# Optimization experiments

Hardware: AMD Instinct MI355X
Metric: run time of the kernel (lower is better)

## Reference

```python
import jax, jax.numpy as jnp
import numpy as np

TOP_K = 2

def setup_inputs() -> dict:
    key = jax.random.key(0)
    ks = jax.random.split(key, 8)
    B, S, H, F, E = 2, 2048, 1024, 2048, 8
    sH = 1.0 / np.sqrt(H)
    sF = 1.0 / np.sqrt(F)
    return {
        "hidden_states": jax.random.normal(ks[0], (B, S, H), jnp.float32),
        "gate_w": jax.random.normal(ks[1], (E, H), jnp.float32) * sH,
        "w_up": jax.random.normal(ks[2], (E, H, F), jnp.float32) * sH,
        "w_gate": jax.random.normal(ks[3], (E, H, F), jnp.float32) * sH,
        "w_down": jax.random.normal(ks[4], (E, F, H), jnp.float32) * sF,
        "b_up": jnp.zeros((E, F), jnp.float32),
        "b_gate": jnp.zeros((E, F), jnp.float32),
        "b_down": jnp.zeros((E, H), jnp.float32),
    }

def reference(hidden_states, gate_w, w_up, w_gate, w_down, b_up, b_gate, b_down):
    # Flatten [B,S,H] -> [N,H]
    H = hidden_states.shape[-1]
    x = hidden_states.reshape(-1, H)                      # [N,H]
    router_logits = x @ gate_w.T                          # [N,E]
    probs = jax.nn.softmax(router_logits.astype(jnp.float32), axis=-1)
    topv, topi = jax.lax.top_k(probs, TOP_K)              # [N,K]
    topv = topv / topv.sum(axis=-1, keepdims=True)
    N, E = router_logits.shape
    # Sparse combine weights: zero except top-k experts (renormalized).
    w_full = jnp.zeros((N, E), probs.dtype).at[jnp.arange(N)[:, None], topi].set(topv)
    w_full = w_full.astype(x.dtype)
    # SwiGLU per expert (dense over E; combine weights zero out non-selected).
    u = jnp.einsum('nh,ehf->nef', x, w_up) + b_up         # [N,E,F]
    v = jnp.einsum('nh,ehf->nef', x, w_gate) + b_gate
    phi = jax.nn.silu(v) * u
    y = jnp.einsum('nef,efh->neh', phi, w_down) + b_down  # [N,E,H]
    out = jnp.einsum('ne,neh->nh', w_full, y)             # [N,H]
    out = out.reshape(hidden_states.shape)
    return out, router_logits.astype(hidden_states.dtype)
```

## Files before the change

kernel.cpp:

```cpp
#include <hip/hip_runtime.h>
#include <hip/hip_bf16.h>
#include <cstdint>
#include <cstddef>

#define N_TOK 4096
#define H_DIM 1024
#define F_DIM 2048
#define E_NUM 8
#define RCAP 10240
#define MAXT 40

typedef __attribute__((ext_vector_type(8))) short bf16x8;
typedef __attribute__((ext_vector_type(4))) float f32x4;

__device__ __forceinline__ float b2f(uint16_t u) {
  return __uint_as_float(((uint32_t)u) << 16);
}
__device__ __forceinline__ uint16_t f2b(float f) {
  uint32_t x = __float_as_uint(f);
  uint32_t r = (x + 0x7fffu + ((x >> 16) & 1u)) >> 16;
  return (uint16_t)r;
}

__device__ __forceinline__ void gl2lds16(const void* g, void* l) {
  __builtin_amdgcn_global_load_lds(
      (const __attribute__((address_space(1))) uint32_t*)g,
      (__attribute__((address_space(3))) uint32_t*)l, 16, 0, 0);
}

__device__ __forceinline__ void stage256(const uint16_t* src, int ldK,
                                         char* lds, int wave, int lane) {
  int u = (lane & 7) ^ (lane >> 3);
  const char* s0 = (const char*)src + u * 16;
  size_t rb = (size_t)ldK * 2;
  int Rb = wave * 32 + (lane >> 3);
  char* d0 = lds + wave * 4096;
  for (int c = 0; c < 4; ++c)
    gl2lds16(s0 + (size_t)(Rb + c * 8) * rb, d0 + c * 1024);
}

__device__ __forceinline__ void stage128(const uint16_t* src, int ldK,
                                         char* lds, int wave, int lane) {
  int u = (lane & 7) ^ (lane >> 3);
  const char* s0 = (const char*)src + u * 16;
  size_t rb = (size_t)ldK * 2;
  int Rb = wave * 16 + (lane >> 3);
  char* d0 = lds + wave * 2048;
  for (int c = 0; c < 2; ++c)
    gl2lds16(s0 + (size_t)(Rb + c * 8) * rb, d0 + c * 1024);
}

__device__ __forceinline__ bf16x8 read_frag(const char* lds, int R, int s,
                                            int q) {
  int unit = ((s << 2) + q) ^ (R & 7);
  return *(const bf16x8*)(lds + R * 128 + unit * 16);
}

__global__ __launch_bounds__(256) void detect_kernel(
    const uint16_t* __restrict__ x, int* __restrict__ flag) {
  __shared__ int cnt;
  if (threadIdx.x == 0) cnt = 0;
  __syncthreads();
  int ok = 0;
  for (int j = 0; j < 16; ++j) {
    uint16_t u = x[threadIdx.x * 16 + j];
    int e = (u >> 7) & 0xff;
    ok += (u == 0 || (e >= 96 && e <= 143)) ? 1 : 0;
  }
  atomicAdd(&cnt, ok);
  __syncthreads();
  if (threadIdx.x == 0) *flag = (cnt >= 3700) ? 1 : 0;
}

__global__ __launch_bounds__(256) void router_kernel(
    const void* __restrict__ xraw, const void* __restrict__ gwraw,
    const int* __restrict__ flag, void* __restrict__ dout,
    int* __restrict__ top_i, float* __restrict__ top_w) {
  int fl = *flag;
  int wave = threadIdx.x >> 6, lane = threadIdx.x & 63;
  int t = blockIdx.x * 4 + wave;
  float xv[16];
  if (fl) {
    const uint16_t* xr = (const uint16_t*)xraw + (size_t)t * H_DIM + lane * 16;
    uint4 a = *(const uint4*)xr;
    uint4 b = *(const uint4*)(xr + 8);
    uint32_t w[8] = {a.x, a.y, a.z, a.w, b.x, b.y, b.z, b.w};
    for (int j = 0; j < 8; ++j) {
      xv[2 * j] = b2f((uint16_t)(w[j] & 0xffff));
      xv[2 * j + 1] = b2f((uint16_t)(w[j] >> 16));
    }
  } else {
    const float* xr = (const float*)xraw + (size_t)t * H_DIM + lane * 16;
    for (int j = 0; j < 4; ++j) {
      float4 v = ((const float4*)xr)[j];
      xv[4 * j] = v.x; xv[4 * j + 1] = v.y;
      xv[4 * j + 2] = v.z; xv[4 * j + 3] = v.w;
    }
  }
  float acc[E_NUM];
  for (int e = 0; e < E_NUM; ++e) {
    float s = 0.f;
    if (fl) {
      const uint16_t* gr =
          (const uint16_t*)gwraw + (size_t)e * H_DIM + lane * 16;
      uint4 a = *(const uint4*)gr;
      uint4 b = *(const uint4*)(gr + 8);
      uint32_t w[8] = {a.x, a.y, a.z, a.w, b.x, b.y, b.z, b.w};
      for (int j = 0; j < 8; ++j) {
        s += xv[2 * j] * b2f((uint16_t)(w[j] & 0xffff));
        s += xv[2 * j + 1] * b2f((uint16_t)(w[j] >> 16));
      }
    } else {
      const float* gr = (const float*)gwraw + (size_t)e * H_DIM + lane * 16;
      for (int j = 0; j < 4; ++j) {
        float4 v = ((const float4*)gr)[j];
        s += xv[4 * j] * v.x + xv[4 * j + 1] * v.y + xv[4 * j + 2] * v.z +
             xv[4 * j + 3] * v.w;
      }
    }
    acc[e] = s;
  }
  for (int off = 32; off >= 1; off >>= 1)
    for (int e = 0; e < E_NUM; ++e)
      acc[e] += __shfl_xor(acc[e], off, 64);
  if (lane < E_NUM) {
    size_t idx = (size_t)N_TOK * H_DIM + (size_t)t * E_NUM + lane;
    if (fl)
      ((uint16_t*)dout)[idx] = f2b(acc[lane]);
    else
      ((float*)dout)[idx] = acc[lane];
  }
  if (lane == 0) {
    int b0 = 0;
    float v0 = acc[0];
    for (int e = 1; e < E_NUM; ++e)
      if (acc[e] > v0) { v0 = acc[e]; b0 = e; }
    int b1 = (b0 == 0) ? 1 : 0;
    float v1 = acc[b1];
    for (int e = 0; e < E_NUM; ++e)
      if (e != b0 && acc[e] > v1) { v1 = acc[e]; b1 = e; }
    float w0 = 1.f / (1.f + expf(v1 - v0));
    top_i[2 * t] = b0; top_i[2 * t + 1] = b1;
    top_w[2 * t] = w0; top_w[2 * t + 1] = 1.f - w0;
  }
}

__global__ __launch_bounds__(1024) void histscan_kernel(
    const int* __restrict__ top_i, int* __restrict__ counts,
    int* __restrict__ bases, int* __restrict__ row_of,
    int* __restrict__ tile_e, int* __restrict__ tile_row,
    int* __restrict__ ntiles) {
  int tid = threadIdx.x;
  int lane = tid & 63, wave = tid >> 6;
  int e_loc[8];
  int c[E_NUM] = {};
  for (int j = 0; j < 8; ++j) {
    int idx = tid * 8 + j;
    int e = top_i[idx];
    e_loc[j] = e;
    c[e]++;
  }
  int inc[E_NUM];
  for (int k = 0; k < E_NUM; ++k) inc[k] = c[k];
  for (int off = 1; off < 64; off <<= 1) {
    for (int k = 0; k < E_NUM; ++k) {
      int v = __shfl_up(inc[k], off, 64);
      if (lane >= off) inc[k] += v;
    }
  }
  __shared__ int wtot[16][E_NUM];
  __shared__ int woff[16][E_NUM];
  __shared__ int base_s[E_NUM];
  if (lane == 63)
    for (int k = 0; k < E_NUM; ++k) wtot[wave][k] = inc[k];
  __syncthreads();
  if (tid < E_NUM) {
    int run = 0;
    for (int w = 0; w < 16; ++w) {
      woff[w][tid] = run;
      run += wtot[w][tid];
    }
    counts[tid] = run;
    wtot[0][tid] = run;
  }
  __syncthreads();
  if (tid == 0) {
    int b = 0, nt = 0;
    for (int e = 0; e < E_NUM; ++e) {
      bases[e] = b;
      base_s[e] = b;
      int cc = wtot[0][e];
      int te = (cc + 255) >> 8;
      for (int j = 0; j < te; ++j) {
        tile_e[nt] = e;
        tile_row[nt] = b + j * 256;
        ++nt;
      }
      b += te << 8;
    }
    *ntiles = nt;
  }
  __syncthreads();
  int run[E_NUM];
  for (int k = 0; k < E_NUM; ++k)
    run[k] = base_s[k] + woff[wave][k] + inc[k] - c[k];
  for (int j = 0; j < 8; ++j) {
    int idx = tid * 8 + j;
    int r = run[e_loc[j]]++;
    row_of[idx] = r;
  }
}

__global__ __launch_bounds__(256) void gather_kernel(
    const void* __restrict__ xraw, const int* __restrict__ flag,
    const int* __restrict__ row_of, uint16_t* __restrict__ Xg) {
  int t = blockIdx.x;
  int rs0 = row_of[2 * t], rs1 = row_of[2 * t + 1];
  uint2 v;
  if (*flag) {
    v = ((const uint2*)((const uint16_t*)xraw + (size_t)t * H_DIM))[threadIdx.x];
  } else {
    float4 f =
        ((const float4*)((const float*)xraw + (size_t)t * H_DIM))[threadIdx.x];
    v.x = (uint32_t)f2b(f.x) | ((uint32_t)f2b(f.y) << 16);
    v.y = (uint32_t)f2b(f.z) | ((uint32_t)f2b(f.w) << 16);
  }
  ((uint2*)(Xg + (size_t)rs0 * H_DIM))[threadIdx.x] = v;
  ((uint2*)(Xg + (size_t)rs1 * H_DIM))[threadIdx.x] = v;
}

__global__ __launch_bounds__(256) void transpose_kernel(
    const void* __restrict__ W, const int* __restrict__ flag,
    uint16_t* __restrict__ Wt, int K, int N) {
  int e = blockIdx.z;
  int n0 = blockIdx.x * 64, k0 = blockIdx.y * 64;
  __shared__ __align__(16) uint16_t tile[64][72];
  size_t ebase = (size_t)e * K * N;
  uint16_t* Wout = Wt + ebase;
  int fl = *flag;
  int r = threadIdx.x >> 3;
  int c = (threadIdx.x & 7) * 8;
  if (fl) {
    const uint16_t* Win = (const uint16_t*)W + ebase;
    for (int it = 0; it < 2; ++it) {
      int row = r + it * 32;
      uint4 v = *(const uint4*)(Win + (size_t)(k0 + row) * N + n0 + c);
      *(uint4*)&tile[row][c] = v;
    }
  } else {
    const float* Win = (const float*)W + ebase;
    for (int it = 0; it < 2; ++it) {
      int row = r + it * 32;
      const float* p = Win + (size_t)(k0 + row) * N + n0 + c;
      float4 a = ((const float4*)p)[0];
      float4 b = ((const float4*)p)[1];
      uint16_t* tp = &tile[row][c];
      tp[0] = f2b(a.x); tp[1] = f2b(a.y); tp[2] = f2b(a.z); tp[3] = f2b(a.w);
      tp[4] = f2b(b.x); tp[5] = f2b(b.y); tp[6] = f2b(b.z); tp[7] = f2b(b.w);
    }
  }
  __syncthreads();
  for (int it = 0; it < 2; ++it) {
    int n = r + it * 32;
    uint4 o;
    o.x = (uint32_t)tile[c + 0][n] | ((uint32_t)tile[c + 1][n] << 16);
    o.y = (uint32_t)tile[c + 2][n] | ((uint32_t)tile[c + 3][n] << 16);
    o.z = (uint32_t)tile[c + 4][n] | ((uint32_t)tile[c + 5][n] << 16);
    o.w = (uint32_t)tile[c + 6][n] | ((uint32_t)tile[c + 7][n] << 16);
    *(uint4*)(Wout + (size_t)(n0 + n) * K + k0 + c) = o;
  }
}

__global__ __launch_bounds__(512, 2) void gemm_upgate(
    const uint16_t* __restrict__ Xg,
    const uint16_t* __restrict__ WtU, const uint16_t* __restrict__ WtG,
    const void* __restrict__ buRaw, const void* __restrict__ bgRaw,
    const int* __restrict__ flag, const int* __restrict__ tile_e,
    const int* __restrict__ tile_row, const int* __restrict__ ntiles,
    uint16_t* __restrict__ phi) {
  int ty = blockIdx.y;
  if (ty >= *ntiles) return;
  int e = tile_e[ty];
  int r0 = tile_row[ty];
  int n0 = blockIdx.x * 128;
  const uint16_t* A = Xg + (size_t)r0 * H_DIM;
  const uint16_t* BU = WtU + (size_t)e * F_DIM * H_DIM + (size_t)n0 * H_DIM;
  const uint16_t* BG = WtG + (size_t)e * F_DIM * H_DIM + (size_t)n0 * H_DIM;

  __shared__ __align__(16) char lA[2][256 * 128];
  __shared__ __align__(16) char lBu[2][128 * 128];
  __shared__ __align__(16) char lBg[2][128 * 128];

  int tid = threadIdx.x;
  int wave = tid >> 6, lane = tid & 63;
  int wm = wave >> 1, wn = wave & 1;
  int q = lane >> 4, mr = lane & 15;

  f32x4 accU[4][4] = {};
  f32x4 accG[4][4] = {};

  stage256(A, H_DIM, lA[0], wave, lane);
  stage128(BU, H_DIM, lBu[0], wave, lane);
  stage128(BG, H_DIM, lBg[0], wave, lane);

  for (int k0 = 0; k0 < H_DIM; k0 += 64) {
    int cur = (k0 >> 6) & 1;
    __syncthreads();
    if (k0 + 64 < H_DIM) {
      stage256(A + k0 + 64, H_DIM, lA[cur ^ 1], wave, lane);
      stage128(BU + k0 + 64, H_DIM, lBu[cur ^ 1], wave, lane);
      stage128(BG + k0 + 64, H_DIM, lBg[cur ^ 1], wave, lane);
    }
    const char* pA = lA[cur];
    const char* pU = lBu[cur];
    const char* pG = lBg[cur];
    for (int s = 0; s < 2; ++s) {
      bf16x8 af[4], bu[4], bg[4];
      for (int mt = 0; mt < 4; ++mt)
        af[mt] = read_frag(pA, wm * 64 + mt * 16 + mr, s, q);
      for (int nt = 0; nt < 4; ++nt) {
        bu[nt] = read_frag(pU, wn * 64 + nt * 16 + mr, s, q);
        bg[nt] = read_frag(pG, wn * 64 + nt * 16 + mr, s, q);
      }
      for (int mt = 0; mt < 4; ++mt)
        for (int nt = 0; nt < 4; ++nt) {
          accU[mt][nt] = __builtin_amdgcn_mfma_f32_16x16x32_bf16(
              af[mt], bu[nt], accU[mt][nt], 0, 0, 0);
          accG[mt][nt] = __builtin_amdgcn_mfma_f32_16x16x32_bf16(
              af[mt], bg[nt], accG[mt][nt], 0, 0, 0);
        }
    }
  }

  int fl = *flag;
  int rb_ = r0 + wm * 64;
  int cb_ = n0 + wn * 64;
  for (int nt = 0; nt < 4; ++nt) {
    int col = cb_ + nt * 16 + mr;
    float bu_v, bg_v;
    if (fl) {
      bu_v = b2f(((const uint16_t*)buRaw)[(size_t)e * F_DIM + col]);
      bg_v = b2f(((const uint16_t*)bgRaw)[(size_t)e * F_DIM + col]);
    } else {
      bu_v = ((const float*)buRaw)[(size_t)e * F_DIM + col];
      bg_v = ((const float*)bgRaw)[(size_t)e * F_DIM + col];
    }
    for (int mt = 0; mt < 4; ++mt) {
      int r = rb_ + mt * 16 + q * 4;
      for (int rg = 0; rg < 4; ++rg) {
        float u = accU[mt][nt][rg] + bu_v;
        float v = accG[mt][nt][rg] + bg_v;
        float s = v / (1.f + expf(-v));
        phi[(size_t)(r + rg) * F_DIM + col] = f2b(s * u);
      }
    }
  }
}

__global__ __launch_bounds__(512, 2) void gemm_down(
    const uint16_t* __restrict__ phi, const uint16_t* __restrict__ WtD,
    const void* __restrict__ bdRaw, const int* __restrict__ flag,
    const int* __restrict__ tile_e, const int* __restrict__ tile_row,
    const int* __restrict__ ntiles, float* __restrict__ Yrows) {
  int ty = blockIdx.y;
  if (ty >= *ntiles) return;
  int e = tile_e[ty];
  int r0 = tile_row[ty];
  int n0 = blockIdx.x * 256;
  const uint16_t* A = phi + (size_t)r0 * F_DIM;
  const uint16_t* B = WtD + (size_t)e * H_DIM * F_DIM + (size_t)n0 * F_DIM;

  __shared__ __align__(16) char lA[2][256 * 128];
  __shared__ __align__(16) char lB[2][256 * 128];

  int tid = threadIdx.x;
  int wave = tid >> 6, lane = tid & 63;
  int wm = wave >> 2, wn = wave & 3;
  int q = lane >> 4, mr = lane & 15;

  f32x4 acc[8][4] = {};

  stage256(A, F_DIM, lA[0], wave, lane);
  stage256(B, F_DIM, lB[0], wave, lane);

  for (int k0 = 0; k0 < F_DIM; k0 += 64) {
    int cur = (k0 >> 6) & 1;
    __syncthreads();
    if (k0 + 64 < F_DIM) {
      stage256(A + k0 + 64, F_DIM, lA[cur ^ 1], wave, lane);
      stage256(B + k0 + 64, F_DIM, lB[cur ^ 1], wave, lane);
    }
    const char* pA = lA[cur];
    const char* pB = lB[cur];
    for (int s = 0; s < 2; ++s) {
      bf16x8 af[8], bf[4];
      for (int mt = 0; mt < 8; ++mt)
        af[mt] = read_frag(pA, wm * 128 + mt * 16 + mr, s, q);
      for (int nt = 0; nt < 4; ++nt)
        bf[nt] = read_frag(pB, wn * 64 + nt * 16 + mr, s, q);
      for (int mt = 0; mt < 8; ++mt)
        for (int nt = 0; nt < 4; ++nt)
          acc[mt][nt] = __builtin_amdgcn_mfma_f32_16x16x32_bf16(
              af[mt], bf[nt], acc[mt][nt], 0, 0, 0);
    }
  }

  int fl = *flag;
  int rb_ = r0 + wm * 128;
  int cb_ = n0 + wn * 64;
  for (int nt = 0; nt < 4; ++nt) {
    int col = cb_ + nt * 16 + mr;
    float bd_v = fl ? b2f(((const uint16_t*)bdRaw)[(size_t)e * H_DIM + col])
                    : ((const float*)bdRaw)[(size_t)e * H_DIM + col];
    for (int mt = 0; mt < 8; ++mt) {
      int r = rb_ + mt * 16 + q * 4;
      for (int rg = 0; rg < 4; ++rg)
        Yrows[(size_t)(r + rg) * H_DIM + col] = acc[mt][nt][rg] + bd_v;
    }
  }
}

__global__ __launch_bounds__(256) void combine_kernel(
    const float* __restrict__ Y, const int* __restrict__ row_of,
    const float* __restrict__ top_w, const int* __restrict__ flag,
    void* __restrict__ out) {
  int t = blockIdx.x;
  int r0 = row_of[2 * t], r1 = row_of[2 * t + 1];
  float w0 = top_w[2 * t], w1 = top_w[2 * t + 1];
  int i = threadIdx.x;
  float4 a = ((const float4*)(Y + (size_t)r0 * H_DIM))[i];
  float4 b = ((const float4*)(Y + (size_t)r1 * H_DIM))[i];
  float4 o;
  o.x = w0 * a.x + w1 * b.x;
  o.y = w0 * a.y + w1 * b.y;
  o.z = w0 * a.z + w1 * b.z;
  o.w = w0 * a.w + w1 * b.w;
  if (*flag) {
    uint2 p;
    p.x = (uint32_t)f2b(o.x) | ((uint32_t)f2b(o.y) << 16);
    p.y = (uint32_t)f2b(o.z) | ((uint32_t)f2b(o.w) << 16);
    ((uint2*)out)[(size_t)t * 256 + i] = p;
  } else {
    ((float4*)out)[(size_t)t * 256 + i] = o;
  }
}

extern "C" void kernel_launch(void* const* d_in, const int* in_sizes, int n_in,
                              void* d_out, int out_size, void* d_ws, size_t ws_size,
                              hipStream_t stream) {
  const void* x = d_in[0];
  const void* gw = d_in[1];
  const void* w_up = d_in[2];
  const void* w_gate = d_in[3];
  const void* w_down = d_in[4];
  const void* b_up = d_in[5];
  const void* b_gate = d_in[6];
  const void* b_down = d_in[7];

  char* ws = (char*)d_ws;
  size_t off = 0;
  auto alloc = [&](size_t bytes) -> void* {
    void* p = ws + off;
    off += (bytes + 255) & ~(size_t)255;
    return p;
  };
  int* counts = (int*)alloc(32);
  int* bases = (int*)alloc(32);
  int* flag = (int*)alloc(32);
  int* ntiles = (int*)alloc(32);
  int* tile_e = (int*)alloc(sizeof(int) * MAXT);
  int* tile_row = (int*)alloc(sizeof(int) * MAXT);
  int* top_i = (int*)alloc(sizeof(int) * N_TOK * 2);
  float* top_w = (float*)alloc(sizeof(float) * N_TOK * 2);
  int* row_of = (int*)alloc(sizeof(int) * N_TOK * 2);
  uint16_t* Xg = (uint16_t*)alloc((size_t)RCAP * H_DIM * 2);
  uint16_t* phi = (uint16_t*)alloc((size_t)RCAP * F_DIM * 2);
  uint16_t* WtU = (uint16_t*)alloc((size_t)E_NUM * H_DIM * F_DIM * 2);
  uint16_t* WtG = (uint16_t*)alloc((size_t)E_NUM * H_DIM * F_DIM * 2);
  float* Yrows = (float*)alloc((size_t)RCAP * H_DIM * sizeof(float));

  detect_kernel<<<1, 256, 0, stream>>>((const uint16_t*)x, flag);
  router_kernel<<<N_TOK / 4, 256, 0, stream>>>(x, gw, flag, d_out, top_i,
                                               top_w);
  histscan_kernel<<<1, 1024, 0, stream>>>(top_i, counts, bases, row_of,
                                          tile_e, tile_row, ntiles);
  gather_kernel<<<N_TOK, 256, 0, stream>>>(x, flag, row_of, Xg);

  transpose_kernel<<<dim3(F_DIM / 64, H_DIM / 64, E_NUM), 256, 0, stream>>>(
      w_up, flag, WtU, H_DIM, F_DIM);
  transpose_kernel<<<dim3(F_DIM / 64, H_DIM / 64, E_NUM), 256, 0, stream>>>(
      w_gate, flag, WtG, H_DIM, F_DIM);

  gemm_upgate<<<dim3(F_DIM / 128, MAXT), 512, 0, stream>>>(
      Xg, WtU, WtG, b_up, b_gate, flag, tile_e, tile_row, ntiles, phi);

  transpose_kernel<<<dim3(H_DIM / 64, F_DIM / 64, E_NUM), 256, 0, stream>>>(
      w_down, flag, WtU, F_DIM, H_DIM);
  gemm_down<<<dim3(H_DIM / 256, MAXT), 512, 0, stream>>>(
      phi, WtU, b_down, flag, tile_e, tile_row, ntiles, Yrows);

  combine_kernel<<<N_TOK, 256, 0, stream>>>(Yrows, row_of, top_w, flag, d_out);
}
```

Measured before the change: 455.8 us.

## Shrink MoE GEMM row tiles to 128, drop double buffering, merge up/gate transposes

Expert row tiles shrink from 256 to 128 rows, which cuts padding waste per expert. Both GEMMs move to 256-thread blocks with 128x128 output tiles, so more blocks launch and occupancy can rise. LDS double buffering is removed in favour of single-buffered staging with two barriers per K step, so global loads no longer overlap MFMA work. The up and gate weight transposes are merged into one launch, and the smaller tiles lower per-block reuse of weights.

```diff
diff --git a/kernel.cpp b/kernel.cpp
--- a/kernel.cpp
+++ b/kernel.cpp
@@ -7,8 +7,8 @@
 #define H_DIM 1024
 #define F_DIM 2048
 #define E_NUM 8
-#define RCAP 10240
-#define MAXT 40
+#define RCAP 9216
+#define MAXT 80
 
 typedef __attribute__((ext_vector_type(8))) short bf16x8;
 typedef __attribute__((ext_vector_type(4))) float f32x4;
@@ -28,26 +28,15 @@
       (__attribute__((address_space(3))) uint32_t*)l, 16, 0, 0);
 }
 
-__device__ __forceinline__ void stage256(const uint16_t* src, int ldK,
-                                         char* lds, int wave, int lane) {
+__device__ __forceinline__ void stage_tile(const uint16_t* src, int ldK,
+                                           char* lds, int wave, int lane) {
   int u = (lane & 7) ^ (lane >> 3);
   const char* s0 = (const char*)src + u * 16;
   size_t rb = (size_t)ldK * 2;
   int Rb = wave * 32 + (lane >> 3);
-  char* d0 = lds + wave * 4096;
-  for (int c = 0; c < 4; ++c)
-    gl2lds16(s0 + (size_t)(Rb + c * 8) * rb, d0 + c * 1024);
-}
-
-__device__ __forceinline__ void stage128(const uint16_t* src, int ldK,
-                                         char* lds, int wave, int lane) {
-  int u = (lane & 7) ^ (lane >> 3);
-  const char* s0 = (const char*)src + u * 16;
-  size_t rb = (size_t)ldK * 2;
-  int Rb = wave * 16 + (lane >> 3);
-  char* d0 = lds + wave * 2048;
-  for (int c = 0; c < 2; ++c)
-    gl2lds16(s0 + (size_t)(Rb + c * 8) * rb, d0 + c * 1024);
+  for (int c = 0; c < 4; ++c) {
+    gl2lds16(s0 + (size_t)(Rb + c * 8) * rb, lds + wave * 4096 + c * 1024);
+  }
 }
 
 __device__ __forceinline__ bf16x8 read_frag(const char* lds, int R, int s,
@@ -190,13 +179,13 @@
       bases[e] = b;
       base_s[e] = b;
       int cc = wtot[0][e];
-      int te = (cc + 255) >> 8;
+      int te = (cc + 127) >> 7;
       for (int j = 0; j < te; ++j) {
         tile_e[nt] = e;
-        tile_row[nt] = b + j * 256;
+        tile_row[nt] = b + j * 128;
         ++nt;
       }
-      b += te << 8;
+      b += te << 7;
     }
     *ntiles = nt;
   }
@@ -230,9 +219,13 @@
 }
 
 __global__ __launch_bounds__(256) void transpose_kernel(
-    const void* __restrict__ W, const int* __restrict__ flag,
-    uint16_t* __restrict__ Wt, int K, int N) {
-  int e = blockIdx.z;
+    const void* __restrict__ W0, const void* __restrict__ W1,
+    const int* __restrict__ flag, uint16_t* __restrict__ Wt0,
+    uint16_t* __restrict__ Wt1, int K, int N) {
+  int z = blockIdx.z;
+  int e = z & (E_NUM - 1);
+  const void* W = (z < E_NUM) ? W0 : W1;
+  uint16_t* Wt = (z < E_NUM) ? Wt0 : Wt1;
   int n0 = blockIdx.x * 64, k0 = blockIdx.y * 64;
   __shared__ __align__(16) uint16_t tile[64][72];
   size_t ebase = (size_t)e * K * N;
@@ -271,7 +264,7 @@
   }
 }
 
-__global__ __launch_bounds__(512, 2) void gemm_upgate(
+__global__ __launch_bounds__(256, 2) void gemm_upgate(
     const uint16_t* __restrict__ Xg,
     const uint16_t* __restrict__ WtU, const uint16_t* __restrict__ WtG,
     const void* __restrict__ buRaw, const void* __restrict__ bgRaw,
@@ -287,9 +280,9 @@
   const uint16_t* BU = WtU + (size_t)e * F_DIM * H_DIM + (size_t)n0 * H_DIM;
   const uint16_t* BG = WtG + (size_t)e * F_DIM * H_DIM + (size_t)n0 * H_DIM;
 
-  __shared__ __align__(16) char lA[2][256 * 128];
-  __shared__ __align__(16) char lBu[2][128 * 128];
-  __shared__ __align__(16) char lBg[2][128 * 128];
+  __shared__ __align__(16) char lA[128 * 128];
+  __shared__ __align__(16) char lBu[128 * 128];
+  __shared__ __align__(16) char lBg[128 * 128];
 
   int tid = threadIdx.x;
   int wave = tid >> 6, lane = tid & 63;
@@ -299,28 +292,19 @@
   f32x4 accU[4][4] = {};
   f32x4 accG[4][4] = {};
 
-  stage256(A, H_DIM, lA[0], wave, lane);
-  stage128(BU, H_DIM, lBu[0], wave, lane);
-  stage128(BG, H_DIM, lBg[0], wave, lane);
-
   for (int k0 = 0; k0 < H_DIM; k0 += 64) {
-    int cur = (k0 >> 6) & 1;
     __syncthreads();
-    if (k0 + 64 < H_DIM) {
-      stage256(A + k0 + 64, H_DIM, lA[cur ^ 1], wave, lane);
-      stage128(BU + k0 + 64, H_DIM, lBu[cur ^ 1], wave, lane);
-      stage128(BG + k0 + 64, H_DIM, lBg[cur ^ 1], wave, lane);
-    }
-    const char* pA = lA[cur];
-    const char* pU = lBu[cur];
-    const char* pG = lBg[cur];
+    stage_tile(A + k0, H_DIM, lA, wave, lane);
+    stage_tile(BU + k0, H_DIM, lBu, wave, lane);
+    stage_tile(BG + k0, H_DIM, lBg, wave, lane);
+    __syncthreads();
     for (int s = 0; s < 2; ++s) {
       bf16x8 af[4], bu[4], bg[4];
       for (int mt = 0; mt < 4; ++mt)
-        af[mt] = read_frag(pA, wm * 64 + mt * 16 + mr, s, q);
+        af[mt] = read_frag(lA, wm * 64 + mt * 16 + mr, s, q);
       for (int nt = 0; nt < 4; ++nt) {
-        bu[nt] = read_frag(pU, wn * 64 + nt * 16 + mr, s, q);
-        bg[nt] = read_frag(pG, wn * 64 + nt * 16 + mr, s, q);
+        bu[nt] = read_frag(lBu, wn * 64 + nt * 16 + mr, s, q);
+        bg[nt] = read_frag(lBg, wn * 64 + nt * 16 + mr, s, q);
       }
       for (int mt = 0; mt < 4; ++mt)
         for (int nt = 0; nt < 4; ++nt) {
@@ -333,10 +317,10 @@
   }
 
   int fl = *flag;
-  int rb_ = r0 + wm * 64;
-  int cb_ = n0 + wn * 64;
+  int rbase = r0 + wm * 64;
+  int cbase = n0 + wn * 64;
   for (int nt = 0; nt < 4; ++nt) {
-    int col = cb_ + nt * 16 + mr;
+    int col = cbase + nt * 16 + mr;
     float bu_v, bg_v;
     if (fl) {
       bu_v = b2f(((const uint16_t*)buRaw)[(size_t)e * F_DIM + col]);
@@ -346,7 +330,7 @@
       bg_v = ((const float*)bgRaw)[(size_t)e * F_DIM + col];
     }
     for (int mt = 0; mt < 4; ++mt) {
-      int r = rb_ + mt * 16 + q * 4;
+      int r = rbase + mt * 16 + q * 4;
       for (int rg = 0; rg < 4; ++rg) {
         float u = accU[mt][nt][rg] + bu_v;
         float v = accG[mt][nt][rg] + bg_v;
@@ -357,7 +341,7 @@
   }
 }
 
-__global__ __launch_bounds__(512, 2) void gemm_down(
+__global__ __launch_bounds__(256, 3) void gemm_down(
     const uint16_t* __restrict__ phi, const uint16_t* __restrict__ WtD,
     const void* __restrict__ bdRaw, const int* __restrict__ flag,
     const int* __restrict__ tile_e, const int* __restrict__ tile_row,
@@ -366,39 +350,32 @@
   if (ty >= *ntiles) return;
   int e = tile_e[ty];
   int r0 = tile_row[ty];
-  int n0 = blockIdx.x * 256;
+  int n0 = blockIdx.x * 128;
   const uint16_t* A = phi + (size_t)r0 * F_DIM;
   const uint16_t* B = WtD + (size_t)e * H_DIM * F_DIM + (size_t)n0 * F_DIM;
 
-  __shared__ __align__(16) char lA[2][256 * 128];
-  __shared__ __align__(16) char lB[2][256 * 128];
+  __shared__ __align__(16) char lA[128 * 128];
+  __shared__ __align__(16) char lB[128 * 128];
 
   int tid = threadIdx.x;
   int wave = tid >> 6, lane = tid & 63;
-  int wm = wave >> 2, wn = wave & 3;
+  int wm = wave >> 1, wn = wave & 1;
   int q = lane >> 4, mr = lane & 15;
 
-  f32x4 acc[8][4] = {};
-
-  stage256(A, F_DIM, lA[0], wave, lane);
-  stage256(B, F_DIM, lB[0], wave, lane);
+  f32x4 acc[4][4] = {};
 
   for (int k0 = 0; k0 < F_DIM; k0 += 64) {
-    int cur = (k0 >> 6) & 1;
     __syncthreads();
-    if (k0 + 64 < F_DIM) {
-      stage256(A + k0 + 64, F_DIM, lA[cur ^ 1], wave, lane);
-      stage256(B + k0 + 64, F_DIM, lB[cur ^ 1], wave, lane);
-    }
-    const char* pA = lA[cur];
-    const char* pB = lB[cur];
+    stage_tile(A + k0, F_DIM, lA, wave, lane);
+    stage_tile(B + k0, F_DIM, lB, wave, lane);
+    __syncthreads();
     for (int s = 0; s < 2; ++s) {
-      bf16x8 af[8], bf[4];
-      for (int mt = 0; mt < 8; ++mt)
-        af[mt] = read_frag(pA, wm * 128 + mt * 16 + mr, s, q);
+      bf16x8 af[4], bf[4];
+      for (int mt = 0; mt < 4; ++mt)
+        af[mt] = read_frag(lA, wm * 64 + mt * 16 + mr, s, q);
       for (int nt = 0; nt < 4; ++nt)
-        bf[nt] = read_frag(pB, wn * 64 + nt * 16 + mr, s, q);
-      for (int mt = 0; mt < 8; ++mt)
+        bf[nt] = read_frag(lB, wn * 64 + nt * 16 + mr, s, q);
+      for (int mt = 0; mt < 4; ++mt)
         for (int nt = 0; nt < 4; ++nt)
           acc[mt][nt] = __builtin_amdgcn_mfma_f32_16x16x32_bf16(
               af[mt], bf[nt], acc[mt][nt], 0, 0, 0);
@@ -406,14 +383,14 @@
   }
 
   int fl = *flag;
-  int rb_ = r0 + wm * 128;
-  int cb_ = n0 + wn * 64;
+  int rbase = r0 + wm * 64;
+  int cbase = n0 + wn * 64;
   for (int nt = 0; nt < 4; ++nt) {
-    int col = cb_ + nt * 16 + mr;
+    int col = cbase + nt * 16 + mr;
     float bd_v = fl ? b2f(((const uint16_t*)bdRaw)[(size_t)e * H_DIM + col])
                     : ((const float*)bdRaw)[(size_t)e * H_DIM + col];
-    for (int mt = 0; mt < 8; ++mt) {
-      int r = rb_ + mt * 16 + q * 4;
+    for (int mt = 0; mt < 4; ++mt) {
+      int r = rbase + mt * 16 + q * 4;
       for (int rg = 0; rg < 4; ++rg)
         Yrows[(size_t)(r + rg) * H_DIM + col] = acc[mt][nt][rg] + bd_v;
     }
@@ -486,17 +463,15 @@
                                           tile_e, tile_row, ntiles);
   gather_kernel<<<N_TOK, 256, 0, stream>>>(x, flag, row_of, Xg);
 
-  transpose_kernel<<<dim3(F_DIM / 64, H_DIM / 64, E_NUM), 256, 0, stream>>>(
-      w_up, flag, WtU, H_DIM, F_DIM);
-  transpose_kernel<<<dim3(F_DIM / 64, H_DIM / 64, E_NUM), 256, 0, stream>>>(
-      w_gate, flag, WtG, H_DIM, F_DIM);
-
-  gemm_upgate<<<dim3(F_DIM / 128, MAXT), 512, 0, stream>>>(
+  transpose_kernel<<<dim3(F_DIM / 64, H_DIM / 64, 2 * E_NUM), 256, 0,
+                     stream>>>(w_up, w_gate, flag, WtU, WtG, H_DIM, F_DIM);
+
+  gemm_upgate<<<dim3(F_DIM / 128, MAXT), 256, 0, stream>>>(
       Xg, WtU, WtG, b_up, b_gate, flag, tile_e, tile_row, ntiles, phi);
 
   transpose_kernel<<<dim3(H_DIM / 64, F_DIM / 64, E_NUM), 256, 0, stream>>>(
-      w_down, flag, WtU, F_DIM, H_DIM);
-  gemm_down<<<dim3(H_DIM / 256, MAXT), 512, 0, stream>>>(
+      w_down, w_down, flag, WtU, WtU, F_DIM, H_DIM);
+  gemm_down<<<dim3(H_DIM / 128, MAXT), 256, 0, stream>>>(
       phi, WtU, b_down, flag, tile_e, tile_row, ntiles, Yrows);
 
   combine_kernel<<<N_TOK, 256, 0, stream>>>(Yrows, row_of, top_w, flag, d_out);
```

Result: faster. 417.2 us (-8.5%).
